# Performance work log

Hardware: AMD Instinct MI355X
Metric: run time of the kernel (lower is better)

The kernel has to match this reference:

```python
import jax, jax.numpy as jnp
import numpy as np

H = 256
W = 256
RADIUS = 1.5
TAU = 1.0
EPS = 1e-8


def _ndc_grid(h, w):
    ys, xs = jnp.meshgrid(jnp.arange(h, dtype=jnp.float32), jnp.arange(w, dtype=jnp.float32), indexing='ij')
    xs = xs / (w - 1) * 2.0 - 1.0
    ys = ys / (h - 1) * 2.0 - 1.0
    return jnp.stack([xs.ravel(), ys.ravel()], 0)  # [2, N]


def _make_rt(key, b, v):
    # near-identity extrinsics: identity rotation + small random translation
    t = jax.random.normal(key, (b, v, 3), dtype=jnp.float32) * 0.05
    rt = jnp.tile(jnp.eye(4, dtype=jnp.float32), (b, v, 1, 1))
    rt = rt.at[:, :, :3, 3].set(t)
    return rt


def setup_inputs() -> dict:
    key = jax.random.key(0)
    ks = jax.random.split(key, 4)
    B, V, C = 2, 3, 32
    depths = jax.random.uniform(ks[0], (B, V, 1, H, W), jnp.float32, 1.0, 3.0)
    feats = jax.random.normal(ks[1], (B, V, C, H, W), jnp.float32)
    K = jnp.tile(jnp.eye(4, dtype=jnp.float32), (B, 1, 1))
    K = K.at[:, 0, 0].set(1.2).at[:, 1, 1].set(1.2)  # NDC-space focal lengths
    src_RTs = _make_rt(ks[2], B, V)
    src_RTinvs = jnp.linalg.inv(src_RTs)
    dst_RTs = _make_rt(ks[3], B, 1)
    dst_RTinvs = jnp.linalg.inv(dst_RTs)
    return {"depths": depths, "feats": feats, "K": K, "src_RTs": src_RTs,
            "src_RTinvs": src_RTinvs, "dst_RTs": dst_RTs, "dst_RTinvs": dst_RTinvs}


def _view_to_world(depth, K_inv, RTinv):
    # depth: [BV, 1, N] -> world homogeneous coords [BV, 4, N]
    grid = _ndc_grid(H, W)                                      # [2, N]
    xy = grid[None] * depth                                     # [BV, 2, N]
    pc = jnp.concatenate([xy, depth, jnp.ones_like(depth)], 1)  # [BV, 4, N]
    cam = jnp.einsum('bij,bjn->bin', K_inv, pc)
    return jnp.einsum('bij,bjn->bin', RTinv, cam)


def _world_to_view(wrld, K, RT):
    cam = jnp.einsum('bij,bjn->bin', RT, wrld)
    proj = jnp.einsum('bij,bjn->bin', K, cam)
    z = proj[:, 2:3]
    xy = proj[:, 0:2] / (z + EPS)
    xy = jnp.where(z <= 0.0, -10.0, xy)       # invalid points pushed off-screen
    return jnp.concatenate([xy, z], 1)        # [BV, 3, N]


def _splatter(pc, feats, radius):
    # pc: [BV, N, 3] (x_ndc, y_ndc, depth); feats: [BV, C, N]
    BV, N, _ = pc.shape
    C = feats.shape[1]
    x, y, z = pc[..., 0], pc[..., 1], pc[..., 2]
    px = (x + 1.0) * 0.5 * (W - 1)
    py = (y + 1.0) * 0.5 * (H - 1)
    offs = jnp.array([[dy, dx] for dy in (-1, 0, 1) for dx in (-1, 0, 1)], dtype=jnp.float32)
    ix = jnp.round(px)[..., None] + offs[:, 1]     # [BV, N, 9]
    iy = jnp.round(py)[..., None] + offs[:, 0]
    dist = jnp.sqrt((ix - px[..., None]) ** 2 + (iy - py[..., None]) ** 2 + EPS)
    w_r = jnp.maximum(0.0, 1.0 - dist / radius)    # radius-based falloff
    valid = (ix >= 0) & (ix < W) & (iy >= 0) & (iy < H) & (z[..., None] > 0)
    w_d = jnp.exp(-TAU * z)[..., None]             # depth-aware (soft z-buffer) weight
    w = w_r * w_d * valid.astype(w_r.dtype)        # [BV, N, 9]
    idx = iy.astype(jnp.int32).clip(0, H - 1) * W + ix.astype(jnp.int32).clip(0, W - 1)
    flat = (jnp.arange(BV, dtype=jnp.int32)[:, None, None] * (H * W) + idx).reshape(-1)
    w_sum = jax.ops.segment_sum(w.reshape(-1), flat, num_segments=BV * H * W)
    fw = (feats[:, :, :, None] * w[:, None, :, :]).transpose(0, 2, 3, 1).reshape(-1, C)
    f_sum = jax.ops.segment_sum(fw, flat, num_segments=BV * H * W)
    z_sum = jax.ops.segment_sum((z[..., None] * w).reshape(-1), flat, num_segments=BV * H * W)
    out_f = (f_sum / (w_sum[:, None] + EPS)).reshape(BV, H, W, C).transpose(0, 3, 1, 2)
    out_d = (z_sum / (w_sum + EPS)).reshape(BV, 1, H, W)
    return out_f, out_d


def reference(depths, feats, K, src_RTs, src_RTinvs, dst_RTs, dst_RTinvs):
    B, V, C = feats.shape[0], feats.shape[1], feats.shape[2]
    N = H * W
    d = depths.reshape(B * V, 1, N)
    f = feats.reshape(B * V, C, N)
    K_bv = jnp.repeat(K, V, axis=0)
    K_inv_bv = jnp.repeat(jnp.linalg.inv(K), V, axis=0)
    src_rtinv = src_RTinvs.reshape(B * V, 4, 4)
    dst_rt = jnp.repeat(dst_RTs[:, 0], V, axis=0)
    wrld = _view_to_world(d, K_inv_bv, src_rtinv)      # view -> world per source view
    sampler = _world_to_view(wrld, K_bv, dst_rt)       # world -> target view [BV,3,N]
    pc = sampler.transpose(0, 2, 1)                    # [BV, N, 3]
    prj_f, prj_d = _splatter(pc, f, RADIUS)
    return prj_f.reshape(B, V, C, H, W), prj_d.reshape(B, V, 1, H, W)
```

## Files before the change

### kernel.cpp

```cpp
#include <hip/hip_runtime.h>
#include <hip/hip_fp16.h>
#include <math.h>

#define H 256
#define W 256
#define HW (H * W)
#define B 2
#define V 3
#define BV (B * V)
#define C 32
#define RADIUS 1.5f
#define TAU 1.0f
#define EPS 1e-8f

#define NPIX (BV * HW)
#define NBLK (NPIX / 256)

#define GW 258
#define GH 258
#define NCELL (BV * GH * GW)
#define CCAP 8
#define OVF_CAP 65536

__device__ __forceinline__ int swizzle_block(int bid) {
    return (bid & 7) * (NBLK / 8) + (bid >> 3);
}

__global__ void setup_kernel(const float* __restrict__ Kmat,
                             const float* __restrict__ srcRTinv,
                             const float* __restrict__ dstRT,
                             float* __restrict__ Mbuf) {
    int bv = threadIdx.x;
    if (bv >= BV) return;
    int b = bv / V;

    float a[4][8];
    for (int i = 0; i < 4; i++)
        for (int j = 0; j < 4; j++) {
            a[i][j] = Kmat[b * 16 + i * 4 + j];
            a[i][4 + j] = (i == j) ? 1.0f : 0.0f;
        }
    for (int col = 0; col < 4; col++) {
        int piv = col;
        float best = fabsf(a[col][col]);
        for (int r = col + 1; r < 4; r++) {
            float v = fabsf(a[r][col]);
            if (v > best) { best = v; piv = r; }
        }
        if (piv != col) {
            for (int j = 0; j < 8; j++) {
                float t = a[col][j]; a[col][j] = a[piv][j]; a[piv][j] = t;
            }
        }
        float s = 1.0f / a[col][col];
        for (int j = 0; j < 8; j++) a[col][j] *= s;
        for (int r = 0; r < 4; r++) {
            if (r == col) continue;
            float m = a[r][col];
            for (int j = 0; j < 8; j++) a[r][j] -= m * a[col][j];
        }
    }
    float Kinv[16];
    for (int i = 0; i < 4; i++)
        for (int j = 0; j < 4; j++) Kinv[i * 4 + j] = a[i][4 + j];

    float T1[16];
    const float* S = srcRTinv + bv * 16;
    for (int i = 0; i < 4; i++)
        for (int j = 0; j < 4; j++) {
            float acc = 0.0f;
            for (int k = 0; k < 4; k++) acc += S[i * 4 + k] * Kinv[k * 4 + j];
            T1[i * 4 + j] = acc;
        }
    float T2[16];
    const float* D = dstRT + b * 16;
    for (int i = 0; i < 4; i++)
        for (int j = 0; j < 4; j++) {
            float acc = 0.0f;
            for (int k = 0; k < 4; k++) acc += D[i * 4 + k] * T1[k * 4 + j];
            T2[i * 4 + j] = acc;
        }
    const float* Kb = Kmat + b * 16;
    for (int i = 0; i < 4; i++)
        for (int j = 0; j < 4; j++) {
            float acc = 0.0f;
            for (int k = 0; k < 4; k++) acc += Kb[i * 4 + k] * T2[k * 4 + j];
            Mbuf[bv * 16 + i * 4 + j] = acc;
        }
}

__global__ __launch_bounds__(256) void project_fill_kernel(
    const float* __restrict__ depths, const float* __restrict__ Mbuf,
    int* __restrict__ counts, float2* __restrict__ cells,
    int* __restrict__ ovf_cnt, int4* __restrict__ ovf) {
    int gid = swizzle_block(blockIdx.x) * 256 + threadIdx.x;
    int bv = gid >> 16;
    int n = gid & (HW - 1);
    int pxi = n & (W - 1);
    int pyi = n >> 8;

    float xn = (float)pxi * (2.0f / (W - 1)) - 1.0f;
    float yn = (float)pyi * (2.0f / (H - 1)) - 1.0f;
    float d = depths[gid];
    const float* M = Mbuf + bv * 16;
    float X = xn * d, Y = yn * d;
    float p0 = M[0] * X + M[1] * Y + M[2] * d + M[3];
    float p1 = M[4] * X + M[5] * Y + M[6] * d + M[7];
    float z  = M[8] * X + M[9] * Y + M[10] * d + M[11];

    if (!(z > 0.0f)) return;
    float inv = 1.0f / (z + EPS);
    float px = (p0 * inv + 1.0f) * 0.5f * (float)(W - 1);
    float py = (p1 * inv + 1.0f) * 0.5f * (float)(H - 1);
    float rx = rintf(px), ry = rintf(py);
    if (rx < -1.0f || rx > (float)W || ry < -1.0f || ry > (float)H) return;

    int cell = bv * (GH * GW) + ((int)ry + 1) * GW + ((int)rx + 1);
    int slot = atomicAdd(&counts[cell], 1);
    if (slot < CCAP) {
        float2 e;
        e.x = __uint_as_float((unsigned int)n);
        e.y = d;
        cells[(size_t)cell * CCAP + slot] = e;
    } else {
        int o = atomicAdd(ovf_cnt, 1);
        if (o < OVF_CAP) ovf[o] = make_int4(cell, n, __float_as_int(d), 0);
    }
}

__global__ __launch_bounds__(256) void transpose_kernel(
    const float* __restrict__ feats, __half* __restrict__ featsT) {
    __shared__ float sm[C][257];
    int blk = blockIdx.x;
    int bv = blk >> 8;
    int n0 = (blk & 255) << 8;
    int tid = threadIdx.x;
    const float* src = feats + (size_t)bv * C * HW + n0;
#pragma unroll
    for (int c = 0; c < C; c++) sm[c][tid] = src[(size_t)c * HW + tid];
    __syncthreads();
    __half* dst = featsT + ((size_t)bv * HW + n0) * C;
#pragma unroll
    for (int pass = 0; pass < 8; pass++) {
        int nl = pass * 32 + (tid >> 3);
        int c4 = (tid & 7) << 2;
        __half2 lo = __floats2half2_rn(sm[c4][nl], sm[c4 + 1][nl]);
        __half2 hi = __floats2half2_rn(sm[c4 + 2][nl], sm[c4 + 3][nl]);
        uint2 pk;
        pk.x = *(unsigned int*)&lo;
        pk.y = *(unsigned int*)&hi;
        *(uint2*)(dst + (size_t)nl * C + c4) = pk;
    }
}

__global__ __launch_bounds__(256) void gather_kernel(
    const float* __restrict__ Mbuf, const __half* __restrict__ featsT,
    const int* __restrict__ counts, const float2* __restrict__ cells,
    const int* __restrict__ ovf_cnt, const int4* __restrict__ ovf,
    float* __restrict__ out) {
    int gid = swizzle_block(blockIdx.x) * 256 + threadIdx.x;
    int bv = gid >> 16;
    int q = gid & (HW - 1);
    float qx = (float)(q & (W - 1));
    float qy = (float)(q >> 8);

    const float* M = Mbuf + bv * 16;
    float m00 = M[0], m01 = M[1], m02 = M[2],  m03 = M[3];
    float m10 = M[4], m11 = M[5], m12 = M[6],  m13 = M[7];
    float m20 = M[8], m21 = M[9], m22 = M[10], m23 = M[11];

    const __half* fb = featsT + ((size_t)bv << 16) * C;

    float wsum = 0.0f, zwsum = 0.0f;
    float facc[C];
#pragma unroll
    for (int c = 0; c < C; c++) facc[c] = 0.0f;

    auto accumulate = [&](int n, float d) {
        float xn = (float)(n & (W - 1)) * (2.0f / (W - 1)) - 1.0f;
        float yn = (float)(n >> 8)      * (2.0f / (H - 1)) - 1.0f;
        float X = xn * d, Y = yn * d;
        float p0 = m00 * X + m01 * Y + m02 * d + m03;
        float p1 = m10 * X + m11 * Y + m12 * d + m13;
        float z  = m20 * X + m21 * Y + m22 * d + m23;
        float inv = 1.0f / (z + EPS);
        float px = (p0 * inv + 1.0f) * 0.5f * (float)(W - 1);
        float py = (p1 * inv + 1.0f) * 0.5f * (float)(H - 1);
        float ddx = qx - px, ddy = qy - py;
        float dist = sqrtf(ddx * ddx + ddy * ddy + EPS);
        float wr = fmaxf(0.0f, 1.0f - dist * (1.0f / RADIUS));
        if (wr > 0.0f) {
            float w = wr * expf(-TAU * z);
            wsum += w;
            zwsum += z * w;
            const uint4* fp = (const uint4*)(fb + (size_t)n * C);
#pragma unroll
            for (int g = 0; g < 4; g++) {
                uint4 v = fp[g];
                const __half2* h2 = (const __half2*)&v;
#pragma unroll
                for (int k = 0; k < 4; k++) {
                    float2 f2 = __half22float2(h2[k]);
                    facc[g * 8 + 2 * k]     = fmaf(w, f2.x, facc[g * 8 + 2 * k]);
                    facc[g * 8 + 2 * k + 1] = fmaf(w, f2.y, facc[g * 8 + 2 * k + 1]);
                }
            }
        }
    };

    int cbase = bv * (GH * GW);
#pragma unroll
    for (int dy = 0; dy < 3; dy++) {
        int rowbase = cbase + (q / W + dy) * GW + (q & (W - 1));
#pragma unroll
        for (int dx = 0; dx < 3; dx++) {
            int cell = rowbase + dx;
            int cc = counts[cell];
            int m = min(cc, CCAP);
            const float2* e = cells + (size_t)cell * CCAP;
            for (int j = 0; j < m; j++) {
                float2 v = e[j];
                accumulate((int)__float_as_uint(v.x), v.y);
            }
            if (cc > CCAP) {
                int oc = min(*ovf_cnt, OVF_CAP);
                for (int i = 0; i < oc; i++) {
                    int4 t = ovf[i];
                    if (t.x == cell) accumulate(t.y, __int_as_float(t.z));
                }
            }
        }
    }

    float invw = 1.0f / (wsum + EPS);
    float* ob = out + (size_t)bv * C * HW + q;
#pragma unroll
    for (int c = 0; c < C; c++) ob[(size_t)c * HW] = facc[c] * invw;
    out[(size_t)BV * C * HW + gid] = zwsum * invw;
}

extern "C" void kernel_launch(void* const* d_in, const int* in_sizes, int n_in,
                              void* d_out, int out_size, void* d_ws, size_t ws_size,
                              hipStream_t stream) {
    const float* depths   = (const float*)d_in[0];
    const float* feats    = (const float*)d_in[1];
    const float* Kmat     = (const float*)d_in[2];
    const float* srcRTinv = (const float*)d_in[4];
    const float* dstRT    = (const float*)d_in[5];
    float* out = (float*)d_out;

    char* ws = (char*)d_ws;
    size_t off_cells = 0;
    size_t off_featsT = off_cells + (size_t)NCELL * CCAP * 8;
    size_t off_counts = off_featsT + (size_t)NPIX * C * 2;
    size_t off_ovfcnt = off_counts + (size_t)NCELL * 4;
    size_t off_ovf = off_ovfcnt + 16;
    size_t off_M = off_ovf + (size_t)OVF_CAP * 16;
    size_t needed = off_M + (size_t)BV * 16 * 4;

    if (ws_size < needed) {
        hipMemsetAsync(d_out, 0, (size_t)out_size * 4, stream);
        return;
    }

    float2* cells  = (float2*)(ws + off_cells);
    __half* featsT = (__half*)(ws + off_featsT);
    int* counts    = (int*)(ws + off_counts);
    int* ovf_cnt   = (int*)(ws + off_ovfcnt);
    int4* ovf      = (int4*)(ws + off_ovf);
    float* Mbuf    = (float*)(ws + off_M);

    hipMemsetAsync(counts, 0, (size_t)NCELL * 4 + 16, stream);
    setup_kernel<<<1, 64, 0, stream>>>(Kmat, srcRTinv, dstRT, Mbuf);
    project_fill_kernel<<<NBLK, 256, 0, stream>>>(depths, Mbuf, counts, cells,
                                                  ovf_cnt, ovf);
    transpose_kernel<<<NBLK, 256, 0, stream>>>(feats, featsT);
    gather_kernel<<<NBLK, 256, 0, stream>>>(Mbuf, featsT, counts, cells,
                                            ovf_cnt, ovf, out);
}
```

Before: 197.1 us.

## Replace fixed-capacity cell bins with count/scan/fill compact binning and fp32 features

Replaces the fixed 8-slot per-cell buckets and global overflow list with a three-pass count, block-scan allocate, and fill scheme that stores entries compactly. Each entry now caches the projected px, py and z, so the gather kernel skips reprojection and rejects far points early with a squared-distance test. The transposed feature buffer goes from fp16 back to fp32, which removes the precision loss but doubles feature gather traffic. In exchange it adds two extra kernel launches and a second projection pass.

```diff
diff --git a/kernel.cpp b/kernel.cpp
--- a/kernel.cpp
+++ b/kernel.cpp
@@ -1,5 +1,4 @@
 #include <hip/hip_runtime.h>
-#include <hip/hip_fp16.h>
 #include <math.h>
 
 #define H 256
@@ -19,8 +18,7 @@
 #define GW 258
 #define GH 258
 #define NCELL (BV * GH * GW)
-#define CCAP 8
-#define OVF_CAP 65536
+#define NALLOC_BLK ((NCELL + 255) / 256)
 
 __device__ __forceinline__ int swizzle_block(int bid) {
     return (bid & 7) * (NBLK / 8) + (bid >> 3);
@@ -89,47 +87,78 @@
         }
 }
 
-__global__ __launch_bounds__(256) void project_fill_kernel(
-    const float* __restrict__ depths, const float* __restrict__ Mbuf,
-    int* __restrict__ counts, float2* __restrict__ cells,
-    int* __restrict__ ovf_cnt, int4* __restrict__ ovf) {
-    int gid = swizzle_block(blockIdx.x) * 256 + threadIdx.x;
+__device__ __forceinline__ bool proj_cell(int gid,
+                                          const float* __restrict__ depths,
+                                          const float* __restrict__ Mbuf,
+                                          float& px, float& py, float& z,
+                                          int& cell, int& n) {
     int bv = gid >> 16;
-    int n = gid & (HW - 1);
-    int pxi = n & (W - 1);
-    int pyi = n >> 8;
-
-    float xn = (float)pxi * (2.0f / (W - 1)) - 1.0f;
-    float yn = (float)pyi * (2.0f / (H - 1)) - 1.0f;
+    n = gid & (HW - 1);
+    float xn = (float)(n & (W - 1)) * (2.0f / (W - 1)) - 1.0f;
+    float yn = (float)(n >> 8)      * (2.0f / (H - 1)) - 1.0f;
     float d = depths[gid];
     const float* M = Mbuf + bv * 16;
     float X = xn * d, Y = yn * d;
     float p0 = M[0] * X + M[1] * Y + M[2] * d + M[3];
     float p1 = M[4] * X + M[5] * Y + M[6] * d + M[7];
-    float z  = M[8] * X + M[9] * Y + M[10] * d + M[11];
-
-    if (!(z > 0.0f)) return;
+    z = M[8] * X + M[9] * Y + M[10] * d + M[11];
+    if (!(z > 0.0f)) return false;
     float inv = 1.0f / (z + EPS);
-    float px = (p0 * inv + 1.0f) * 0.5f * (float)(W - 1);
-    float py = (p1 * inv + 1.0f) * 0.5f * (float)(H - 1);
+    px = (p0 * inv + 1.0f) * 0.5f * (float)(W - 1);
+    py = (p1 * inv + 1.0f) * 0.5f * (float)(H - 1);
     float rx = rintf(px), ry = rintf(py);
-    if (rx < -1.0f || rx > (float)W || ry < -1.0f || ry > (float)H) return;
-
-    int cell = bv * (GH * GW) + ((int)ry + 1) * GW + ((int)rx + 1);
-    int slot = atomicAdd(&counts[cell], 1);
-    if (slot < CCAP) {
-        float2 e;
-        e.x = __uint_as_float((unsigned int)n);
-        e.y = d;
-        cells[(size_t)cell * CCAP + slot] = e;
-    } else {
-        int o = atomicAdd(ovf_cnt, 1);
-        if (o < OVF_CAP) ovf[o] = make_int4(cell, n, __float_as_int(d), 0);
-    }
+    if (rx < -1.0f || rx > (float)W || ry < -1.0f || ry > (float)H) return false;
+    cell = bv * (GH * GW) + ((int)ry + 1) * GW + ((int)rx + 1);
+    return true;
+}
+
+__global__ __launch_bounds__(256) void count_kernel(
+    const float* __restrict__ depths, const float* __restrict__ Mbuf,
+    int2* __restrict__ meta) {
+    int gid = swizzle_block(blockIdx.x) * 256 + threadIdx.x;
+    float px, py, z; int cell, n;
+    if (!proj_cell(gid, depths, Mbuf, px, py, z, cell, n)) return;
+    atomicAdd(&meta[cell].y, 1);
+}
+
+__global__ __launch_bounds__(256) void alloc_kernel(int2* __restrict__ meta,
+                                                    int* __restrict__ total) {
+    int i = blockIdx.x * 256 + threadIdx.x;
+    int c = (i < NCELL) ? meta[i].y : 0;
+    int lane = threadIdx.x & 63;
+    int wid = threadIdx.x >> 6;
+    int x = c;
+#pragma unroll
+    for (int dlt = 1; dlt < 64; dlt <<= 1) {
+        int y = __shfl_up(x, dlt);
+        if (lane >= dlt) x += y;
+    }
+    __shared__ int wsum[4];
+    __shared__ int wbase[4];
+    __shared__ int bbase;
+    if (lane == 63) wsum[wid] = x;
+    __syncthreads();
+    if (threadIdx.x == 0) {
+        int s0 = wsum[0], s1 = wsum[1], s2 = wsum[2], s3 = wsum[3];
+        wbase[0] = 0; wbase[1] = s0; wbase[2] = s0 + s1; wbase[3] = s0 + s1 + s2;
+        bbase = atomicAdd(total, s0 + s1 + s2 + s3);
+    }
+    __syncthreads();
+    if (i < NCELL) meta[i].x = bbase + wbase[wid] + (x - c);
+}
+
+__global__ __launch_bounds__(256) void fill_kernel(
+    const float* __restrict__ depths, const float* __restrict__ Mbuf,
+    int2* __restrict__ meta, float4* __restrict__ entries) {
+    int gid = swizzle_block(blockIdx.x) * 256 + threadIdx.x;
+    float px, py, z; int cell, n;
+    if (!proj_cell(gid, depths, Mbuf, px, py, z, cell, n)) return;
+    int pos = atomicAdd(&meta[cell].x, 1);
+    entries[pos] = make_float4(px, py, z, __uint_as_float((unsigned int)n));
 }
 
 __global__ __launch_bounds__(256) void transpose_kernel(
-    const float* __restrict__ feats, __half* __restrict__ featsT) {
+    const float* __restrict__ feats, float* __restrict__ featsT) {
     __shared__ float sm[C][257];
     int blk = blockIdx.x;
     int bv = blk >> 8;
@@ -139,94 +168,62 @@
 #pragma unroll
     for (int c = 0; c < C; c++) sm[c][tid] = src[(size_t)c * HW + tid];
     __syncthreads();
-    __half* dst = featsT + ((size_t)bv * HW + n0) * C;
+    float* dst = featsT + ((size_t)bv * HW + n0) * C;
 #pragma unroll
     for (int pass = 0; pass < 8; pass++) {
         int nl = pass * 32 + (tid >> 3);
         int c4 = (tid & 7) << 2;
-        __half2 lo = __floats2half2_rn(sm[c4][nl], sm[c4 + 1][nl]);
-        __half2 hi = __floats2half2_rn(sm[c4 + 2][nl], sm[c4 + 3][nl]);
-        uint2 pk;
-        pk.x = *(unsigned int*)&lo;
-        pk.y = *(unsigned int*)&hi;
-        *(uint2*)(dst + (size_t)nl * C + c4) = pk;
+        float4 v = make_float4(sm[c4][nl], sm[c4 + 1][nl],
+                               sm[c4 + 2][nl], sm[c4 + 3][nl]);
+        *(float4*)(dst + (size_t)nl * C + c4) = v;
     }
 }
 
 __global__ __launch_bounds__(256) void gather_kernel(
-    const float* __restrict__ Mbuf, const __half* __restrict__ featsT,
-    const int* __restrict__ counts, const float2* __restrict__ cells,
-    const int* __restrict__ ovf_cnt, const int4* __restrict__ ovf,
-    float* __restrict__ out) {
+    const float* __restrict__ featsT, const int2* __restrict__ meta,
+    const float4* __restrict__ entries, float* __restrict__ out) {
     int gid = swizzle_block(blockIdx.x) * 256 + threadIdx.x;
     int bv = gid >> 16;
     int q = gid & (HW - 1);
     float qx = (float)(q & (W - 1));
     float qy = (float)(q >> 8);
 
-    const float* M = Mbuf + bv * 16;
-    float m00 = M[0], m01 = M[1], m02 = M[2],  m03 = M[3];
-    float m10 = M[4], m11 = M[5], m12 = M[6],  m13 = M[7];
-    float m20 = M[8], m21 = M[9], m22 = M[10], m23 = M[11];
-
-    const __half* fb = featsT + ((size_t)bv << 16) * C;
+    const float* fb = featsT + ((size_t)bv << 16) * C;
 
     float wsum = 0.0f, zwsum = 0.0f;
     float facc[C];
 #pragma unroll
     for (int c = 0; c < C; c++) facc[c] = 0.0f;
 
-    auto accumulate = [&](int n, float d) {
-        float xn = (float)(n & (W - 1)) * (2.0f / (W - 1)) - 1.0f;
-        float yn = (float)(n >> 8)      * (2.0f / (H - 1)) - 1.0f;
-        float X = xn * d, Y = yn * d;
-        float p0 = m00 * X + m01 * Y + m02 * d + m03;
-        float p1 = m10 * X + m11 * Y + m12 * d + m13;
-        float z  = m20 * X + m21 * Y + m22 * d + m23;
-        float inv = 1.0f / (z + EPS);
-        float px = (p0 * inv + 1.0f) * 0.5f * (float)(W - 1);
-        float py = (p1 * inv + 1.0f) * 0.5f * (float)(H - 1);
-        float ddx = qx - px, ddy = qy - py;
-        float dist = sqrtf(ddx * ddx + ddy * ddy + EPS);
-        float wr = fmaxf(0.0f, 1.0f - dist * (1.0f / RADIUS));
-        if (wr > 0.0f) {
-            float w = wr * expf(-TAU * z);
-            wsum += w;
-            zwsum += z * w;
-            const uint4* fp = (const uint4*)(fb + (size_t)n * C);
-#pragma unroll
-            for (int g = 0; g < 4; g++) {
-                uint4 v = fp[g];
-                const __half2* h2 = (const __half2*)&v;
-#pragma unroll
-                for (int k = 0; k < 4; k++) {
-                    float2 f2 = __half22float2(h2[k]);
-                    facc[g * 8 + 2 * k]     = fmaf(w, f2.x, facc[g * 8 + 2 * k]);
-                    facc[g * 8 + 2 * k + 1] = fmaf(w, f2.y, facc[g * 8 + 2 * k + 1]);
-                }
-            }
-        }
-    };
-
     int cbase = bv * (GH * GW);
 #pragma unroll
     for (int dy = 0; dy < 3; dy++) {
-        int rowbase = cbase + (q / W + dy) * GW + (q & (W - 1));
+        int rowbase = cbase + ((q >> 8) + dy) * GW + (q & (W - 1));
 #pragma unroll
         for (int dx = 0; dx < 3; dx++) {
-            int cell = rowbase + dx;
-            int cc = counts[cell];
-            int m = min(cc, CCAP);
-            const float2* e = cells + (size_t)cell * CCAP;
-            for (int j = 0; j < m; j++) {
-                float2 v = e[j];
-                accumulate((int)__float_as_uint(v.x), v.y);
-            }
-            if (cc > CCAP) {
-                int oc = min(*ovf_cnt, OVF_CAP);
-                for (int i = 0; i < oc; i++) {
-                    int4 t = ovf[i];
-                    if (t.x == cell) accumulate(t.y, __int_as_float(t.z));
+            int2 m2 = meta[rowbase + dx];
+            int cnt = m2.y;
+            const float4* e = entries + (m2.x - cnt);
+            for (int j = 0; j < cnt; j++) {
+                float4 v = e[j];
+                float ddx = qx - v.x, ddy = qy - v.y;
+                float d2 = ddx * ddx + ddy * ddy + EPS;
+                if (d2 < RADIUS * RADIUS) {
+                    float dist = sqrtf(d2);
+                    float wr = fmaxf(0.0f, 1.0f - dist * (1.0f / RADIUS));
+                    float w = wr * expf(-TAU * v.z);
+                    wsum += w;
+                    zwsum += v.z * w;
+                    int n = (int)__float_as_uint(v.w);
+                    const float4* fp = (const float4*)(fb + (size_t)n * C);
+#pragma unroll
+                    for (int g = 0; g < 8; g++) {
+                        float4 f = fp[g];
+                        facc[g * 4 + 0] = fmaf(w, f.x, facc[g * 4 + 0]);
+                        facc[g * 4 + 1] = fmaf(w, f.y, facc[g * 4 + 1]);
+                        facc[g * 4 + 2] = fmaf(w, f.z, facc[g * 4 + 2]);
+                        facc[g * 4 + 3] = fmaf(w, f.w, facc[g * 4 + 3]);
+                    }
                 }
             }
         }
@@ -250,12 +247,11 @@
     float* out = (float*)d_out;
 
     char* ws = (char*)d_ws;
-    size_t off_cells = 0;
-    size_t off_featsT = off_cells + (size_t)NCELL * CCAP * 8;
-    size_t off_counts = off_featsT + (size_t)NPIX * C * 2;
-    size_t off_ovfcnt = off_counts + (size_t)NCELL * 4;
-    size_t off_ovf = off_ovfcnt + 16;
-    size_t off_M = off_ovf + (size_t)OVF_CAP * 16;
+    size_t off_featsT = 0;
+    size_t off_entries = off_featsT + (size_t)NPIX * C * 4;
+    size_t off_meta = off_entries + (size_t)NPIX * 16;
+    size_t off_total = off_meta + (size_t)NCELL * 8;
+    size_t off_M = off_total + 16;
     size_t needed = off_M + (size_t)BV * 16 * 4;
 
     if (ws_size < needed) {
@@ -263,18 +259,17 @@
         return;
     }
 
-    float2* cells  = (float2*)(ws + off_cells);
-    __half* featsT = (__half*)(ws + off_featsT);
-    int* counts    = (int*)(ws + off_counts);
-    int* ovf_cnt   = (int*)(ws + off_ovfcnt);
-    int4* ovf      = (int4*)(ws + off_ovf);
-    float* Mbuf    = (float*)(ws + off_M);
-
-    hipMemsetAsync(counts, 0, (size_t)NCELL * 4 + 16, stream);
+    float* featsT   = (float*)(ws + off_featsT);
+    float4* entries = (float4*)(ws + off_entries);
+    int2* meta      = (int2*)(ws + off_meta);
+    int* total      = (int*)(ws + off_total);
+    float* Mbuf     = (float*)(ws + off_M);
+
+    hipMemsetAsync(meta, 0, (size_t)NCELL * 8 + 16, stream);
     setup_kernel<<<1, 64, 0, stream>>>(Kmat, srcRTinv, dstRT, Mbuf);
-    project_fill_kernel<<<NBLK, 256, 0, stream>>>(depths, Mbuf, counts, cells,
-                                                  ovf_cnt, ovf);
+    count_kernel<<<NBLK, 256, 0, stream>>>(depths, Mbuf, meta);
+    alloc_kernel<<<NALLOC_BLK, 256, 0, stream>>>(meta, total);
+    fill_kernel<<<NBLK, 256, 0, stream>>>(depths, Mbuf, meta, entries);
     transpose_kernel<<<NBLK, 256, 0, stream>>>(feats, featsT);
-    gather_kernel<<<NBLK, 256, 0, stream>>>(Mbuf, featsT, counts, cells,
-                                            ovf_cnt, ovf, out);
-}
+    gather_kernel<<<NBLK, 256, 0, stream>>>(featsT, meta, entries, out);
+}
```

Result: slower. 271.3 us (+37.7%).
